# Kernel optimization log

Hardware: AMD Instinct MI355X
Metric: run time of the kernel (lower is better)

## Reference

```python
import jax, jax.numpy as jnp
import numpy as np

B, L, C, H, W = 2, 3, 64, 32, 32
DI, N, DT_RANK, K = 128, 16, 4, 4  # d_inner=2*C, d_state, dt_rank=ceil(C/16), 4 scan dirs


def setup_inputs() -> dict:
    key = jax.random.key(0)
    ks = iter(jax.random.split(key, 48))
    nrm = lambda shape, s=0.02: jax.random.normal(next(ks), shape, jnp.float32) * s
    return {
        "image_sequence": jax.random.normal(next(ks), (B, L, C, H, W), jnp.float32),
        "difficult_zone": jax.random.normal(next(ks), (B, C, H, W), jnp.float32),
        "sigma": jax.random.uniform(next(ks), (B, C, H, W), jnp.float32),
        # LayerNorm2d applied to each frame
        "norm_g": jnp.ones((C,)), "norm_b": jnp.zeros((C,)),
        # ConvolutionalResBlock (in=3C -> out=C), GroupNorm(num_groups=1)
        "gn1_g": jnp.ones((3 * C,)), "gn1_b": jnp.zeros((3 * C,)),
        "conv1_w": nrm((C, 3 * C, 3, 3)), "conv1_b": jnp.zeros((C,)),
        "gn2_g": jnp.ones((C,)), "gn2_b": jnp.zeros((C,)),
        "conv2_w": nrm((C, C, 3, 3)), "conv2_b": jnp.zeros((C,)),
        "skip_w": nrm((C, 3 * C, 1, 1)), "skip_b": jnp.zeros((C,)),
        # VSSBlock pre-norms
        "ln1_g": jnp.ones((C,)), "ln1_b": jnp.zeros((C,)),
        "ln2_g": jnp.ones((C,)), "ln2_b": jnp.zeros((C,)),
        # SS2D
        "in_proj_w": nrm((2 * DI, C)),
        "dwconv_w": nrm((DI, 1, 3, 3)), "dwconv_b": jnp.zeros((DI,)),
        "x_proj_w": nrm((K, DT_RANK + 2 * N, DI)),
        "dt_proj_w": nrm((K, DI, DT_RANK), 0.1),
        "dt_proj_b": jnp.log(jnp.expm1(jnp.full((K, DI), 0.01, jnp.float32))),
        "A_logs": jnp.log(jnp.tile(jnp.arange(1, N + 1, dtype=jnp.float32), (K * DI, 1))),
        "Ds": jnp.ones((K * DI,)),
        "out_norm_g": jnp.ones((DI,)), "out_norm_b": jnp.zeros((DI,)),
        "out_proj_w": nrm((C, DI)),
        # Mlp (hidden = C)
        "fc1_w": nrm((C, C)), "fc1_b": jnp.zeros((C,)),
        "fc2_w": nrm((C, C)), "fc2_b": jnp.zeros((C,)),
    }


def _ln(x, g, b, eps=1e-5):  # layernorm over last axis
    m = x.mean(-1, keepdims=True)
    v = x.var(-1, keepdims=True)
    return (x - m) * jax.lax.rsqrt(v + eps) * g + b


def _ln2d(x, g, b, eps=1e-6):  # per-pixel channel layernorm, NCHW
    m = x.mean(1, keepdims=True)
    v = x.var(1, keepdims=True)
    return (x - m) * jax.lax.rsqrt(v + eps) * g[None, :, None, None] + b[None, :, None, None]


def _gn1(x, g, b, eps=1e-5):  # GroupNorm(num_groups=1), NCHW
    m = x.mean((1, 2, 3), keepdims=True)
    v = x.var((1, 2, 3), keepdims=True)
    return (x - m) * jax.lax.rsqrt(v + eps) * g[None, :, None, None] + b[None, :, None, None]


def _conv(x, w, b, pad):
    y = jax.lax.conv_general_dilated(x, w, (1, 1), [(pad, pad), (pad, pad)],
                                     dimension_numbers=("NCHW", "OIHW", "NCHW"))
    return y + b[None, :, None, None]


def _forward(image_sequence, difficult_zone, sigma, norm_g, norm_b, gn1_g, gn1_b,
             conv1_w, conv1_b, gn2_g, gn2_b, conv2_w, conv2_b, skip_w, skip_b,
             ln1_g, ln1_b, ln2_g, ln2_b, in_proj_w, dwconv_w, dwconv_b, x_proj_w,
             dt_proj_w, dt_proj_b, A_logs, Ds, out_norm_g, out_norm_b, out_proj_w,
             fc1_w, fc1_b, fc2_w, fc2_b):
    b, l, c, h, w = image_sequence.shape
    bl, L2 = b * l, h * w
    # fold frame loop into batch (identical math per frame in the torch loop)
    frames = _ln2d(image_sequence.reshape(bl, c, h, w), norm_g, norm_b)
    dz = jnp.broadcast_to(difficult_zone[:, None], (b, l, c, h, w)).reshape(bl, c, h, w)
    sg = jnp.broadcast_to(sigma[:, None], (b, l, c, h, w)).reshape(bl, c, h, w)
    x = jnp.concatenate([dz, frames, sg], axis=1)  # [bl, 3c, h, w]
    # channel compressor: pre-act conv res block
    hdn = _conv(jax.nn.silu(_gn1(x, gn1_g, gn1_b)), conv1_w, conv1_b, 1)
    hdn = _conv(jax.nn.silu(_gn1(hdn, gn2_g, gn2_b)), conv2_w, conv2_b, 1)
    x = hdn + _conv(x, skip_w, skip_b, 0)          # [bl, c, h, w]
    x = x.transpose(0, 2, 3, 1)                    # [bl, h, w, c]
    # --- VSSBlock (pre-norm): x = x + SS2D(LN(x)) ---
    xn = _ln(x, ln1_g, ln1_b)
    xz = xn @ in_proj_w.T                          # [bl,h,w,2*DI]
    xc, z = jnp.split(xz, 2, axis=-1)
    xc = xc.transpose(0, 3, 1, 2)                  # [bl, DI, h, w]
    xc = jax.lax.conv_general_dilated(xc, dwconv_w, (1, 1), [(1, 1), (1, 1)],
                                      dimension_numbers=("NCHW", "OIHW", "NCHW"),
                                      feature_group_count=DI) + dwconv_b[None, :, None, None]
    xc = jax.nn.silu(xc)
    # 4-direction scan inputs (HW, WH, and their reverses)
    xf = xc.reshape(bl, DI, L2)
    xt = xc.transpose(0, 1, 3, 2).reshape(bl, DI, L2)
    xs = jnp.stack([xf, xt], axis=1)
    xs = jnp.concatenate([xs, jnp.flip(xs, axis=-1)], axis=1)  # [bl, 4, DI, L2]
    x_dbl = jnp.einsum("bkdl,kcd->bkcl", xs, x_proj_w)
    dts, Bs, Cs = jnp.split(x_dbl, [DT_RANK, DT_RANK + N], axis=2)
    dts = jnp.einsum("bkrl,kdr->bkdl", dts, dt_proj_w) + dt_proj_b[None, :, :, None]
    dts = jax.nn.softplus(dts)                     # [bl, 4, DI, L2]
    A = -jnp.exp(A_logs).reshape(K, DI, N)
    dA = jnp.exp(dts[..., None] * A[None, :, :, None, :])            # [bl,4,DI,L2,N]
    dBu = dts[..., None] * Bs.transpose(0, 1, 3, 2)[:, :, None] * xs[..., None]
    a_t = dA.transpose(3, 0, 1, 2, 4)              # [L2, bl, 4, DI, N]
    bu_t = dBu.transpose(3, 0, 1, 2, 4)
    c_t = Cs.transpose(3, 0, 1, 2)                 # [L2, bl, 4, N]

    def step(hid, inp):
        a_i, bu_i, c_i = inp
        hid = a_i * hid + bu_i
        return hid, jnp.einsum("bkdn,bkn->bkd", hid, c_i)

    h0 = jnp.zeros((bl, K, DI, N), xs.dtype)
    _, ys = jax.lax.scan(step, h0, (a_t, bu_t, c_t))                 # [L2, bl, 4, DI]
    ys = ys.transpose(1, 2, 3, 0) + xs * Ds.reshape(K, DI)[None, :, :, None]
    inv = jnp.flip(ys[:, 2:4], axis=-1)
    y = (ys[:, 0] + inv[:, 0]
         + ys[:, 1].reshape(bl, DI, w, h).transpose(0, 1, 3, 2).reshape(bl, DI, L2)
         + inv[:, 1].reshape(bl, DI, w, h).transpose(0, 1, 3, 2).reshape(bl, DI, L2))
    y = _ln(y.transpose(0, 2, 1), out_norm_g, out_norm_b).reshape(bl, h, w, DI)
    y = y * jax.nn.silu(z)
    x = x + y @ out_proj_w.T
    # --- x = x + Mlp(LN(x)) ---
    xn = _ln(x, ln2_g, ln2_b)
    x = x + (jax.nn.gelu(xn @ fc1_w.T + fc1_b, approximate=False) @ fc2_w.T + fc2_b)
    return x.transpose(0, 3, 1, 2).reshape(b, l, c, h, w)


def reference(image_sequence, difficult_zone, sigma, norm_g, norm_b, gn1_g, gn1_b,
              conv1_w, conv1_b, gn2_g, gn2_b, conv2_w, conv2_b, skip_w, skip_b,
              ln1_g, ln1_b, ln2_g, ln2_b, in_proj_w, dwconv_w, dwconv_b, x_proj_w,
              dt_proj_w, dt_proj_b, A_logs, Ds, out_norm_g, out_norm_b, out_proj_w,
              fc1_w, fc1_b, fc2_w, fc2_b):
    return _forward(image_sequence, difficult_zone, sigma, norm_g, norm_b, gn1_g, gn1_b,
                    conv1_w, conv1_b, gn2_g, gn2_b, conv2_w, conv2_b, skip_w, skip_b,
                    ln1_g, ln1_b, ln2_g, ln2_b, in_proj_w, dwconv_w, dwconv_b, x_proj_w,
                    dt_proj_w, dt_proj_b, A_logs, Ds, out_norm_g, out_norm_b, out_proj_w,
                    fc1_w, fc1_b, fc2_w, fc2_b)
```

## Files before the change

### kernel.cpp

```cpp
#include <hip/hip_runtime.h>
#include <math.h>

#define BL    6
#define CCH   64
#define C3    192
#define L2    1024
#define DIC   128
#define NST   16
#define K4    4
#define PSTR  1088
#define NCH   32

#define LOG2E 1.44269504088896340736f
#define LN2C  0.69314718055994530942f

__device__ __forceinline__ float fexp(float x){ return __builtin_amdgcn_exp2f(x*LOG2E); }
__device__ __forceinline__ float fsilu(float x){ return x / (1.f + fexp(-x)); }
__device__ __forceinline__ float fsoftplus(float x){
  if (x > 20.f) return x;
  return __builtin_amdgcn_logf(1.f + fexp(x)) * LN2C;
}
__device__ __forceinline__ float fgelu(float x){
  return 0.5f*x*(1.f + erff(x*0.70710678118654752440f));
}

__global__ __launch_bounds__(256) void k_ln2d(const float* __restrict__ img,
    const float* __restrict__ dz, const float* __restrict__ sg,
    const float* __restrict__ g, const float* __restrict__ b, float* __restrict__ x3c,
    float* __restrict__ psum1, float* __restrict__ psq1){
  __shared__ float ps[4][64], pq[4][64];
  int s = blockIdx.x >> 4;
  int lane = threadIdx.x & 63;
  int cg = threadIdx.x >> 6;
  int p = ((blockIdx.x & 15) << 6) + lane;
  int bsmp = s/3;
  const float* fr = img + (size_t)s*CCH*L2;
  float vals[16]; float sm=0.f, sq=0.f;
  #pragma unroll
  for (int j=0;j<16;++j){
    int c = cg*16+j;
    float v = fr[c*L2+p];
    vals[j]=v; sm+=v; sq+=v*v;
  }
  ps[cg][lane]=sm; pq[cg][lane]=sq;
  __syncthreads();
  sm = ps[0][lane]+ps[1][lane]+ps[2][lane]+ps[3][lane];
  sq = pq[0][lane]+pq[1][lane]+pq[2][lane]+pq[3][lane];
  float mean = sm*(1.f/CCH); float var = sq*(1.f/CCH) - mean*mean;
  float rs = rsqrtf(var + 1e-6f);
  float* o = x3c + (size_t)s*C3*L2;
  const float* dzp = dz + (size_t)bsmp*CCH*L2;
  const float* sgp = sg + (size_t)bsmp*CCH*L2;
  float gsm=0.f, gsq=0.f;
  #pragma unroll
  for (int j=0;j<16;++j){
    int c = cg*16+j;
    float dzv = dzp[c*L2+p];
    float nv  = (vals[j]-mean)*rs*g[c] + b[c];
    float sgv = sgp[c*L2+p];
    o[c*L2+p] = dzv;
    o[(CCH+c)*L2+p] = nv;
    o[(2*CCH+c)*L2+p] = sgv;
    gsm += dzv+nv+sgv; gsq += dzv*dzv+nv*nv+sgv*sgv;
  }
  for (int m=1;m<64;m<<=1){ gsm+=__shfl_xor(gsm,m,64); gsq+=__shfl_xor(gsq,m,64); }
  __syncthreads();
  if (lane==0){ ps[cg][0]=gsm; pq[cg][0]=gsq; }
  __syncthreads();
  if (threadIdx.x==0){
    atomicAdd(psum1+s, ps[0][0]+ps[1][0]+ps[2][0]+ps[3][0]);
    atomicAdd(psq1 +s, pq[0][0]+pq[1][0]+pq[2][0]+pq[3][0]);
  }
}

__global__ __launch_bounds__(256) void k_gnact_pad(const float* __restrict__ x,
    const float* __restrict__ psum, const float* __restrict__ psq,
    const float* __restrict__ g, const float* __restrict__ b,
    int ch, float inv_n, float eps, float* __restrict__ out){
  int bx = blockIdx.x;
  int s = bx / ch; int c = bx % ch;
  int tid = threadIdx.x;
  float mean = psum[s]*inv_n;
  float var = psq[s]*inv_n - mean*mean;
  float rs = rsqrtf(var + eps);
  float gc = g[c]*rs; float bc = b[c] - mean*rs*g[c];
  float4 v = *(const float4*)(x + (size_t)bx*1024 + tid*4);
  float4 o; o.x = fsilu(v.x*gc+bc); o.y = fsilu(v.y*gc+bc);
  o.z = fsilu(v.z*gc+bc); o.w = fsilu(v.w*gc+bc);
  float* pl = out + (size_t)bx*PSTR;
  *(float4*)(pl + 32 + tid*4) = o;
  float4 z4 = make_float4(0.f,0.f,0.f,0.f);
  if (tid < 8)  *(float4*)(pl + tid*4) = z4;
  else if (tid < 16) *(float4*)(pl + 1056 + (tid-8)*4) = z4;
}

__device__ __forceinline__ void conv_row_acc(float4& a0, float4& a1, float4 mid, float lf, float rt,
    const float* wp0, const float* wp1){
  float w0=wp0[0], w1=wp0[1], w2=wp0[2];
  a0.x = fmaf(w0,lf,   fmaf(w1,mid.x, fmaf(w2,mid.y, a0.x)));
  a0.y = fmaf(w0,mid.x,fmaf(w1,mid.y, fmaf(w2,mid.z, a0.y)));
  a0.z = fmaf(w0,mid.y,fmaf(w1,mid.z, fmaf(w2,mid.w, a0.z)));
  a0.w = fmaf(w0,mid.z,fmaf(w1,mid.w, fmaf(w2,rt,    a0.w)));
  float v0=wp1[0], v1=wp1[1], v2=wp1[2];
  a1.x = fmaf(v0,lf,   fmaf(v1,mid.x, fmaf(v2,mid.y, a1.x)));
  a1.y = fmaf(v0,mid.x,fmaf(v1,mid.y, fmaf(v2,mid.z, a1.y)));
  a1.z = fmaf(v0,mid.y,fmaf(v1,mid.z, fmaf(v2,mid.w, a1.z)));
  a1.w = fmaf(v0,mid.z,fmaf(v1,mid.w, fmaf(v2,rt,    a1.w)));
}

__device__ __forceinline__ void conv_ci_body(float4 m0, float4 m1, float4 m2, int q,
    const float* wp0, const float* wp1, float4& a0, float4& a1){
  float lf0=__shfl_up(m0.w,1,64), rt0=__shfl_down(m0.x,1,64);
  float lf1=__shfl_up(m1.w,1,64), rt1=__shfl_down(m1.x,1,64);
  float lf2=__shfl_up(m2.w,1,64), rt2=__shfl_down(m2.x,1,64);
  if (q==0){ lf0=0.f; lf1=0.f; lf2=0.f; }
  if (q==7){ rt0=0.f; rt1=0.f; rt2=0.f; }
  conv_row_acc(a0,a1,m0,lf0,rt0, wp0+0, wp1+0);
  conv_row_acc(a0,a1,m1,lf1,rt1, wp0+3, wp1+3);
  conv_row_acc(a0,a1,m2,lf2,rt2, wp0+6, wp1+6);
}

__global__ __launch_bounds__(256) void k_conv1_split(const float* __restrict__ xact,
    const float* __restrict__ w, float* __restrict__ part){
  int bx = blockIdx.x; int kk = bx&7; int cop=(bx>>3)&31; int s=bx>>8;
  int co0 = cop*2, co1 = co0+1;
  int tid = threadIdx.x; int row = tid>>3; int q = tid&7; int col0 = q*4;
  float4 a0 = make_float4(0.f,0.f,0.f,0.f);
  float4 a1 = make_float4(0.f,0.f,0.f,0.f);
  int ci0 = kk*24;
  const float* pl = xact + ((size_t)s*C3 + ci0)*PSTR + row*32 + col0;
  const float* wp0 = w + (size_t)(co0*C3 + ci0)*9;
  const float* wp1 = w + (size_t)(co1*C3 + ci0)*9;
  float4 m0 = *(const float4*)(pl);
  float4 m1 = *(const float4*)(pl+32);
  float4 m2 = *(const float4*)(pl+64);
  #pragma unroll 2
  for (int i=0;i<24;++i){
    const float* pn = pl + (i<23 ? PSTR : 0);
    float4 n0 = *(const float4*)(pn);
    float4 n1 = *(const float4*)(pn+32);
    float4 n2 = *(const float4*)(pn+64);
    conv_ci_body(m0,m1,m2,q, wp0, wp1, a0, a1);
    wp0 += 9; wp1 += 9; pl = pn; m0=n0; m1=n1; m2=n2;
  }
  float* pp = part + (size_t)kk*(BL*CCH*L2) + ((size_t)s*CCH+co0)*L2 + row*32+col0;
  *(float4*)pp = a0;
  *(float4*)(pp+L2) = a1;
}

__global__ __launch_bounds__(256) void k_reduce1(const float* __restrict__ part,
    const float* __restrict__ bias, float* __restrict__ h1,
    float* __restrict__ psum2, float* __restrict__ psq2){
  int co = blockIdx.x & 63; int s = blockIdx.x >> 6;
  size_t ofs = ((size_t)s*CCH+co)*L2 + threadIdx.x*4;
  const size_t stride = (size_t)BL*CCH*L2;
  float4 acc = *(const float4*)(part + ofs);
  #pragma unroll
  for (int kk=1;kk<8;++kk){
    float4 r = *(const float4*)(part + (size_t)kk*stride + ofs);
    acc.x += r.x; acc.y += r.y; acc.z += r.z; acc.w += r.w;
  }
  float bv = bias[co];
  acc.x += bv; acc.y += bv; acc.z += bv; acc.w += bv;
  *(float4*)(h1 + ofs) = acc;
  float sm = acc.x+acc.y+acc.z+acc.w;
  float sq = acc.x*acc.x+acc.y*acc.y+acc.z*acc.z+acc.w*acc.w;
  for (int m=1;m<64;m<<=1){ sm+=__shfl_xor(sm,m,64); sq+=__shfl_xor(sq,m,64); }
  __shared__ float s_sm[4], s_sq[4];
  int wv = threadIdx.x>>6;
  if ((threadIdx.x&63)==0){ s_sm[wv]=sm; s_sq[wv]=sq; }
  __syncthreads();
  if (threadIdx.x==0){
    atomicAdd(psum2+s, s_sm[0]+s_sm[1]+s_sm[2]+s_sm[3]);
    atomicAdd(psq2 +s, s_sq[0]+s_sq[1]+s_sq[2]+s_sq[3]);
  }
}

__global__ __launch_bounds__(256) void k_conv2_split(const float* __restrict__ xact2,
    const float* __restrict__ x3c, const float* __restrict__ w2,
    const float* __restrict__ wsk, float* __restrict__ part){
  int t = blockIdx.x; int role = t % 3; t /= 3;
  int cop = t & 31; int s = t >> 5;
  int co0 = cop*2, co1 = co0+1;
  int tid = threadIdx.x; int row = tid>>3; int q = tid&7; int col0 = q*4;
  int p = row*32+col0;
  float4 a0 = make_float4(0.f,0.f,0.f,0.f);
  float4 a1 = make_float4(0.f,0.f,0.f,0.f);
  if (role < 2){
    int ci0 = role*32;
    const float* pl = xact2 + ((size_t)s*CCH + ci0)*PSTR + row*32 + col0;
    const float* wp0 = w2 + (size_t)(co0*CCH + ci0)*9;
    const float* wp1 = w2 + (size_t)(co1*CCH + ci0)*9;
    float4 m0 = *(const float4*)(pl);
    float4 m1 = *(const float4*)(pl+32);
    float4 m2 = *(const float4*)(pl+64);
    #pragma unroll 2
    for (int i=0;i<32;++i){
      const float* pn = pl + (i<31 ? PSTR : 0);
      float4 n0 = *(const float4*)(pn);
      float4 n1 = *(const float4*)(pn+32);
      float4 n2 = *(const float4*)(pn+64);
      conv_ci_body(m0,m1,m2,q, wp0, wp1, a0, a1);
      wp0 += 9; wp1 += 9; pl = pn; m0=n0; m1=n1; m2=n2;
    }
  } else {
    const float* x3 = x3c + (size_t)s*C3*L2 + p;
    #pragma unroll 4
    for (int ci=0; ci<C3; ++ci){
      float4 v = *(const float4*)(x3 + (size_t)ci*L2);
      float ws0 = wsk[co0*C3+ci], ws1 = wsk[co1*C3+ci];
      a0.x = fmaf(ws0,v.x,a0.x); a0.y = fmaf(ws0,v.y,a0.y); a0.z = fmaf(ws0,v.z,a0.z); a0.w = fmaf(ws0,v.w,a0.w);
      a1.x = fmaf(ws1,v.x,a1.x); a1.y = fmaf(ws1,v.y,a1.y); a1.z = fmaf(ws1,v.z,a1.z); a1.w = fmaf(ws1,v.w,a1.w);
    }
  }
  float* pp = part + (size_t)role*(BL*CCH*L2) + ((size_t)s*CCH+co0)*L2 + p;
  *(float4*)pp = a0;
  *(float4*)(pp+L2) = a1;
}

__global__ __launch_bounds__(256) void k_reduce2(const float* __restrict__ part,
    const float* __restrict__ b2, const float* __restrict__ bsk,
    float* __restrict__ xp, float* __restrict__ x_cmaj){
  int co = blockIdx.x & 63; int s = blockIdx.x >> 6;
  int p = threadIdx.x*4;
  size_t ofs = ((size_t)s*CCH+co)*L2 + p;
  const size_t stride = (size_t)BL*CCH*L2;
  float4 r0 = *(const float4*)(part + ofs);
  float4 r1 = *(const float4*)(part + stride + ofs);
  float4 r2 = *(const float4*)(part + 2*stride + ofs);
  float bv = b2[co]+bsk[co];
  float4 o;
  o.x = r0.x+r1.x+r2.x+bv;
  o.y = r0.y+r1.y+r2.y+bv;
  o.z = r0.z+r1.z+r2.z+bv;
  o.w = r0.w+r1.w+r2.w+bv;
  *(float4*)(x_cmaj + ofs) = o;
  float* xpb = xp + ((size_t)s*L2 + p)*CCH + co;
  xpb[0] = o.x; xpb[CCH] = o.y; xpb[2*CCH] = o.z; xpb[3*CCH] = o.w;
}

__global__ __launch_bounds__(256) void k_ln1_inproj(const float* __restrict__ xp,
    const float* __restrict__ g, const float* __restrict__ b, const float* __restrict__ W,
    float* __restrict__ xc, float* __restrict__ z_t){
  __shared__ float xn_s[64*65];
  int bx = blockIdx.x; int oq = bx & 3; int pg = (bx>>2)&15; int s = bx>>6;
  int p0 = pg*64;
  int tid = threadIdx.x; int wv = __builtin_amdgcn_readfirstlane(tid>>6); int lane = tid&63;
  for (int j=0;j<16;++j){
    int pl = wv*16 + j; int p = p0 + pl;
    float v = xp[((size_t)s*L2 + p)*CCH + lane];
    float sm = v, sq = v*v;
    for (int m=1;m<64;m<<=1){ sm += __shfl_xor(sm,m,64); sq += __shfl_xor(sq,m,64); }
    float mean = sm*(1.f/64.f); float var = sq*(1.f/64.f) - mean*mean;
    float rs = rsqrtf(var + 1e-5f);
    xn_s[pl*65 + lane] = (v-mean)*rs*g[lane] + b[lane];
  }
  __syncthreads();
  int px_l = tid & 63;
  int og = __builtin_amdgcn_readfirstlane(tid >> 6);
  int o0 = oq*64 + og*16;
  float acc[16];
  #pragma unroll
  for (int oi=0;oi<16;++oi) acc[oi]=0.f;
  for (int c=0;c<64;++c){
    float xv = xn_s[px_l*65 + c];
    #pragma unroll
    for (int oi=0;oi<16;++oi) acc[oi] = fmaf(W[(o0+oi)*64 + c], xv, acc[oi]);
  }
  int p = p0 + px_l;
  if (oq < 2){
    #pragma unroll
    for (int oi=0;oi<16;++oi) xc[((size_t)s*DIC + o0 + oi)*L2 + p] = acc[oi];
  } else {
    #pragma unroll
    for (int oi=0;oi<16;++oi) z_t[((size_t)s*DIC + (o0-128) + oi)*L2 + p] = acc[oi];
  }
}

__global__ __launch_bounds__(256) void k_dwconv(const float* __restrict__ xc,
    const float* __restrict__ w, const float* __restrict__ bias, float* __restrict__ xconv){
  int bx = blockIdx.x; int dch = bx & 127; int s = bx >> 7;
  int tid = threadIdx.x; int row = tid>>3; int q = tid&7; int col0 = q*4;
  const float* xr = xc + ((size_t)s*DIC+dch)*L2;
  const float* wp = w + dch*9;
  float bv = bias[dch];
  float4 acc = make_float4(bv,bv,bv,bv);
  #pragma unroll
  for (int dy=-1;dy<=1;++dy){
    int r = row+dy;
    float4 mid = make_float4(0.f,0.f,0.f,0.f);
    if (0<=r && r<32) mid = *(const float4*)(xr + r*32 + col0);
    float lf = __shfl_up(mid.w,1,64); if(q==0) lf=0.f;
    float rt = __shfl_down(mid.x,1,64); if(q==7) rt=0.f;
    float w0=wp[(dy+1)*3], w1=wp[(dy+1)*3+1], w2=wp[(dy+1)*3+2];
    acc.x = fmaf(w0,lf,   fmaf(w1,mid.x, fmaf(w2,mid.y, acc.x)));
    acc.y = fmaf(w0,mid.x,fmaf(w1,mid.y, fmaf(w2,mid.z, acc.y)));
    acc.z = fmaf(w0,mid.y,fmaf(w1,mid.z, fmaf(w2,mid.w, acc.z)));
    acc.w = fmaf(w0,mid.z,fmaf(w1,mid.w, fmaf(w2,rt,    acc.w)));
  }
  acc.x = fsilu(acc.x); acc.y = fsilu(acc.y); acc.z = fsilu(acc.z); acc.w = fsilu(acc.w);
  *(float4*)(xconv + ((size_t)s*DIC+dch)*L2 + row*32+col0) = acc;
}

__global__ __launch_bounds__(256) void k_xproj_dt(const float* __restrict__ xconv,
    const float* __restrict__ W, const float* __restrict__ dtw, const float* __restrict__ dtb,
    float* __restrict__ dtp, float* __restrict__ Bp, float* __restrict__ Cp,
    float* __restrict__ u_t){
  __shared__ float smem[128*68];
  int bx = blockIdx.x; int pg = bx & 15; int sk = bx >> 4;
  int k = sk & 3; int s = sk >> 2;
  int tid = threadIdx.x;
  for (int i = tid; i < 128*16; i += 256){
    int dr = i>>4; int j4 = (i&15)*4;
    float4 v = *(const float4*)(xconv + ((size_t)(s*DIC + dr))*L2 + pg*64 + j4);
    *(float4*)&smem[dr*68 + j4] = v;
  }
  __syncthreads();
  if (k == 0){
    float* ub = u_t + ((size_t)(s*L2) + pg*64)*DIC;
    for (int i = tid; i < 64*128; i += 256){
      int px2 = i>>7; int dd = i&127;
      ub[(size_t)px2*DIC + dd] = smem[dd*68 + px2];
    }
  }
  int px = tid & 63;
  int cgrp = __builtin_amdgcn_readfirstlane(tid >> 6);
  int c0 = cgrp*9;
  const float* wb = W + (size_t)(k*36 + c0)*DIC;
  float acc[9];
  #pragma unroll
  for (int ci=0;ci<9;++ci) acc[ci]=0.f;
  for (int d=0; d<DIC; ++d){
    float xv = smem[d*68 + px];
    #pragma unroll
    for (int ci=0;ci<9;++ci) acc[ci] = fmaf(wb[ci*DIC+d], xv, acc[ci]);
  }
  __syncthreads();
  #pragma unroll
  for (int ci=0;ci<9;++ci) smem[(c0+ci)*68 + px] = acc[ci];
  __syncthreads();
  int d = tid & 127; int half = tid >> 7;
  float w0 = dtw[(k*DIC+d)*4+0], w1 = dtw[(k*DIC+d)*4+1];
  float w2 = dtw[(k*DIC+d)*4+2], w3 = dtw[(k*DIC+d)*4+3];
  float bb = dtb[k*DIC+d];
  float* dout = dtp + ((size_t)sk*L2 + pg*64)*DIC + d;
  for (int pp = half*32; pp < half*32+32; ++pp){
    float r0 = smem[0*68+pp], r1 = smem[1*68+pp], r2 = smem[2*68+pp], r3 = smem[3*68+pp];
    float val = fsoftplus(fmaf(w0,r0,fmaf(w1,r1,fmaf(w2,r2,fmaf(w3,r3,bb)))));
    dout[(size_t)pp*DIC] = val;
  }
  float* Bb = Bp + ((size_t)sk*L2 + pg*64)*NST;
  float* Cb = Cp + ((size_t)sk*L2 + pg*64)*NST;
  for (int i = tid; i < 1024; i += 256){
    int pp = i>>4; int n = i&15;
    Bb[pp*NST + n] = smem[(4+n)*68 + pp];
    Cb[pp*NST + n] = smem[(20+n)*68 + pp];
  }
}

__device__ __forceinline__ int scan_pix32(int ch, int j, int k){
  if (k==0) return ch*32 + j;
  if (k==1) return j*32 + ch;
  if (k==2) return 1023 - (ch*32 + j);
  return 1023 - (j*32 + ch);
}

struct StepB { float dtv, uv; float4 B0,B1,B2,B3; };
__device__ __forceinline__ StepB loadB(const float* db, const float* ub, const float* Bb, int p){
  StepB r;
  r.dtv = db[(size_t)p*DIC]; r.uv = ub[(size_t)p*DIC];
  const float* bp = Bb + p*NST;
  r.B0 = *(const float4*)bp; r.B1 = *(const float4*)(bp+4);
  r.B2 = *(const float4*)(bp+8); r.B3 = *(const float4*)(bp+12);
  return r;
}

__global__ __launch_bounds__(256,2) void k_scan_part3(const float* __restrict__ dtp,
    const float* __restrict__ u_t, const float* __restrict__ Bp,
    const float* __restrict__ A_logs, float* __restrict__ hend, float* __restrict__ prodA){
  int bx = blockIdx.x; int chp = bx & 15; int sk = bx >> 4;
  int k = sk & 3; int s = sk >> 2;
  int tid = threadIdx.x; int d = tid & 127; int ch = chp*2 + (tid>>7);
  float aco[16];
  {
    const float* ab = A_logs + (size_t)(k*DIC+d)*NST;
    #pragma unroll
    for (int n=0;n<16;++n) aco[n] = -LOG2E * fexp(ab[n]);
  }
  float h[16], Pr[16];
  #pragma unroll
  for (int n=0;n<16;++n){ h[n]=0.f; Pr[n]=1.f; }
  const float* db = dtp + (size_t)sk*L2*DIC + d;
  const float* ub = u_t + (size_t)s*L2*DIC + d;
  const float* Bb = Bp + (size_t)sk*L2*NST;
  StepB cur = loadB(db, ub, Bb, scan_pix32(ch, 0, k));
  #pragma unroll 4
  for (int j=0;j<32;++j){
    StepB nxt;
    if (j < 31) nxt = loadB(db, ub, Bb, scan_pix32(ch, j+1, k));
    float tv = cur.dtv*cur.uv;
    #define PSTEP(NI, BV) { float a_ = __builtin_amdgcn_exp2f(cur.dtv*aco[NI]); \
      h[NI] = fmaf(a_, h[NI], tv*(BV)); Pr[NI] *= a_; }
    PSTEP(0,cur.B0.x) PSTEP(1,cur.B0.y) PSTEP(2,cur.B0.z) PSTEP(3,cur.B0.w)
    PSTEP(4,cur.B1.x) PSTEP(5,cur.B1.y) PSTEP(6,cur.B1.z) PSTEP(7,cur.B1.w)
    PSTEP(8,cur.B2.x) PSTEP(9,cur.B2.y) PSTEP(10,cur.B2.z) PSTEP(11,cur.B2.w)
    PSTEP(12,cur.B3.x) PSTEP(13,cur.B3.y) PSTEP(14,cur.B3.z) PSTEP(15,cur.B3.w)
    #undef PSTEP
    cur = nxt;
  }
  size_t base = ((size_t)(sk*NCH + ch)*DIC + d)*NST;
  #pragma unroll
  for (int q4=0;q4<4;++q4){
    *(float4*)(hend + base + q4*4)  = make_float4(h[q4*4],h[q4*4+1],h[q4*4+2],h[q4*4+3]);
    *(float4*)(prodA + base + q4*4) = make_float4(Pr[q4*4],Pr[q4*4+1],Pr[q4*4+2],Pr[q4*4+3]);
  }
}

__global__ __launch_bounds__(256) void k_scan_fix3(const float* __restrict__ hend,
    float* prodA_Hin){
  int t = blockIdx.x*256 + threadIdx.x;
  int n = t & 15; int d = (t>>4) & 127; int sk = t >> 11;
  float H = 0.f;
  for (int ch=0; ch<NCH; ++ch){
    size_t idx = ((size_t)(sk*NCH + ch)*DIC + d)*NST + n;
    float pa = prodA_Hin[idx];
    float he = hend[idx];
    prodA_Hin[idx] = H;
    H = fmaf(pa, H, he);
  }
}

__global__ __launch_bounds__(256,2) void k_scan_y3(const float* __restrict__ dtp,
    const float* __restrict__ u_t, const float* __restrict__ Bp, const float* __restrict__ Cp,
    const float* __restrict__ A_logs, const float* __restrict__ Ds,
    const float* __restrict__ Hin, float* __restrict__ ys_t){
  int bx = blockIdx.x; int chp = bx & 15; int sk = bx >> 4;
  int k = sk & 3; int s = sk >> 2;
  int tid = threadIdx.x; int d = tid & 127; int ch = chp*2 + (tid>>7);
  float aco[16];
  {
    const float* ab = A_logs + (size_t)(k*DIC+d)*NST;
    #pragma unroll
    for (int n=0;n<16;++n) aco[n] = -LOG2E * fexp(ab[n]);
  }
  float Dv = Ds[k*DIC+d];
  float h[16];
  size_t hbase = ((size_t)(sk*NCH + ch)*DIC + d)*NST;
  #pragma unroll
  for (int q4=0;q4<4;++q4){
    float4 hv = *(const float4*)(Hin + hbase + q4*4);
    h[q4*4]=hv.x; h[q4*4+1]=hv.y; h[q4*4+2]=hv.z; h[q4*4+3]=hv.w;
  }
  const float* db = dtp + (size_t)sk*L2*DIC + d;
  const float* ub = u_t + (size_t)s*L2*DIC + d;
  const float* Bb = Bp + (size_t)sk*L2*NST;
  const float* Cb = Cp + (size_t)sk*L2*NST;
  float* yb = ys_t + (size_t)sk*L2*DIC + d;
  int pcur = scan_pix32(ch, 0, k);
  StepB cur = loadB(db, ub, Bb, pcur);
  float4 Cc0 = *(const float4*)(Cb + pcur*NST);
  float4 Cc1 = *(const float4*)(Cb + pcur*NST + 4);
  float4 Cc2 = *(const float4*)(Cb + pcur*NST + 8);
  float4 Cc3 = *(const float4*)(Cb + pcur*NST + 12);
  #pragma unroll 4
  for (int j=0;j<32;++j){
    StepB nxt; float4 Cn0, Cn1, Cn2, Cn3; int pn = pcur;
    if (j < 31){
      pn = scan_pix32(ch, j+1, k);
      nxt = loadB(db, ub, Bb, pn);
      Cn0 = *(const float4*)(Cb + pn*NST);
      Cn1 = *(const float4*)(Cb + pn*NST + 4);
      Cn2 = *(const float4*)(Cb + pn*NST + 8);
      Cn3 = *(const float4*)(Cb + pn*NST + 12);
    }
    float tv = cur.dtv*cur.uv;
    float y0=0.f, y1=0.f, y2=0.f, y3=0.f;
    #define YSTEP(NI, BV, CV, YA) { float a_ = __builtin_amdgcn_exp2f(cur.dtv*aco[NI]); \
      h[NI] = fmaf(a_, h[NI], tv*(BV)); YA = fmaf(h[NI], (CV), YA); }
    YSTEP(0,cur.B0.x,Cc0.x,y0) YSTEP(1,cur.B0.y,Cc0.y,y1) YSTEP(2,cur.B0.z,Cc0.z,y2) YSTEP(3,cur.B0.w,Cc0.w,y3)
    YSTEP(4,cur.B1.x,Cc1.x,y0) YSTEP(5,cur.B1.y,Cc1.y,y1) YSTEP(6,cur.B1.z,Cc1.z,y2) YSTEP(7,cur.B1.w,Cc1.w,y3)
    YSTEP(8,cur.B2.x,Cc2.x,y0) YSTEP(9,cur.B2.y,Cc2.y,y1) YSTEP(10,cur.B2.z,Cc2.z,y2) YSTEP(11,cur.B2.w,Cc2.w,y3)
    YSTEP(12,cur.B3.x,Cc3.x,y0) YSTEP(13,cur.B3.y,Cc3.y,y1) YSTEP(14,cur.B3.z,Cc3.z,y2) YSTEP(15,cur.B3.w,Cc3.w,y3)
    #undef YSTEP
    yb[(size_t)pcur*DIC] = fmaf(cur.uv, Dv, (y0+y1)+(y2+y3));
    cur = nxt; Cc0 = Cn0; Cc1 = Cn1; Cc2 = Cn2; Cc3 = Cn3; pcur = pn;
  }
}

__global__ __launch_bounds__(256) void k_combine_outproj(const float* __restrict__ ys_t,
    const float* __restrict__ z_t, const float* __restrict__ g, const float* __restrict__ b,
    const float* __restrict__ W, const float* __restrict__ x_cmaj, float* __restrict__ xv){
  __shared__ float yt[128*17];
  int s = blockIdx.x >> 6; int pg = blockIdx.x & 63;
  int tid = threadIdx.x;
  int wv = __builtin_amdgcn_readfirstlane(tid>>6); int lane = tid&63;
  int d0 = lane, d1 = lane+64;
  for (int i=0;i<4;++i){
    int px = i*4 + wv; int p = pg*16 + px;
    const float* yb = ys_t + ((size_t)(s*4)*L2 + p)*DIC;
    float ya = yb[d0] + yb[(size_t)L2*DIC + d0] + yb[(size_t)2*L2*DIC + d0] + yb[(size_t)3*L2*DIC + d0];
    float yc = yb[d1] + yb[(size_t)L2*DIC + d1] + yb[(size_t)2*L2*DIC + d1] + yb[(size_t)3*L2*DIC + d1];
    float sm = ya+yc, sq = ya*ya+yc*yc;
    for (int m=1;m<64;m<<=1){ sm+=__shfl_xor(sm,m,64); sq+=__shfl_xor(sq,m,64); }
    float mean = sm*(1.f/128.f); float var = sq*(1.f/128.f)-mean*mean;
    float rs = rsqrtf(var + 1e-5f);
    float yn0 = (ya-mean)*rs*g[d0] + b[d0];
    float yn1 = (yc-mean)*rs*g[d1] + b[d1];
    float zv0 = z_t[((size_t)s*DIC+d0)*L2 + p];
    float zv1 = z_t[((size_t)s*DIC+d1)*L2 + p];
    yt[d0*17 + px] = yn0 * fsilu(zv0);
    yt[d1*17 + px] = yn1 * fsilu(zv1);
  }
  __syncthreads();
  int px = tid & 15; int cg = tid >> 4;
  int c0 = cg*4;
  float a0=0.f,a1=0.f,a2=0.f,a3=0.f;
  for (int d=0; d<DIC; ++d){
    float yv = yt[d*17 + px];
    a0 = fmaf(W[(c0+0)*DIC + d], yv, a0);
    a1 = fmaf(W[(c0+1)*DIC + d], yv, a1);
    a2 = fmaf(W[(c0+2)*DIC + d], yv, a2);
    a3 = fmaf(W[(c0+3)*DIC + d], yv, a3);
  }
  int p = pg*16 + px;
  size_t base = ((size_t)s*CCH + c0)*L2 + p;
  xv[base]      = x_cmaj[base]      + a0;
  xv[base+L2]   = x_cmaj[base+L2]   + a1;
  xv[base+2*L2] = x_cmaj[base+2*L2] + a2;
  xv[base+3*L2] = x_cmaj[base+3*L2] + a3;
}

__global__ __launch_bounds__(256) void k_mlp(const float* __restrict__ xv_in,
    const float* __restrict__ g, const float* __restrict__ b,
    const float* __restrict__ w1, const float* __restrict__ b1,
    const float* __restrict__ w2, const float* __restrict__ b2, float* __restrict__ out){
  __shared__ float xt[64*33];
  __shared__ float ts[32*65];
  int s = blockIdx.x >> 5; int p0 = (blockIdx.x & 31)*32;
  int tid = threadIdx.x; int px = tid & 31; int cg = tid >> 5;
  #pragma unroll
  for (int j=0;j<8;++j){
    int c = cg*8 + j;
    xt[c*33 + px] = xv_in[((size_t)s*CCH + c)*L2 + p0 + px];
  }
  __syncthreads();
  float sm=0.f, sq=0.f;
  for (int c=0;c<64;++c){ float v = xt[c*33+px]; sm+=v; sq+=v*v; }
  float mean = sm*(1.f/64.f);
  float rs = rsqrtf(sq*(1.f/64.f) - mean*mean + 1e-5f);
  int o0 = cg*8;
  float t[8];
  #pragma unroll
  for (int oi=0;oi<8;++oi) t[oi] = b1[o0+oi];
  for (int c=0;c<64;++c){
    float xn = (xt[c*33+px]-mean)*rs*g[c] + b[c];
    #pragma unroll
    for (int oi=0;oi<8;++oi) t[oi] = fmaf(xn, w1[(o0+oi)*64 + c], t[oi]);
  }
  #pragma unroll
  for (int oi=0;oi<8;++oi) ts[px*65 + o0+oi] = fgelu(t[oi]);
  __syncthreads();
  int c0 = cg*8;
  float acc[8];
  #pragma unroll
  for (int ci=0;ci<8;++ci) acc[ci] = xt[(c0+ci)*33+px] + b2[c0+ci];
  for (int o=0;o<64;++o){
    float tv = ts[px*65 + o];
    #pragma unroll
    for (int ci=0;ci<8;++ci) acc[ci] = fmaf(tv, w2[(c0+ci)*64 + o], acc[ci]);
  }
  #pragma unroll
  for (int ci=0;ci<8;++ci) out[((size_t)s*CCH + c0+ci)*L2 + p0 + px] = acc[ci];
}

extern "C" void kernel_launch(void* const* d_in, const int* in_sizes, int n_in,
                              void* d_out, int out_size, void* d_ws, size_t ws_size,
                              hipStream_t stream){
  (void)in_sizes; (void)n_in; (void)out_size; (void)ws_size;
  const float* img      = (const float*)d_in[0];
  const float* dz       = (const float*)d_in[1];
  const float* sg       = (const float*)d_in[2];
  const float* norm_g   = (const float*)d_in[3];
  const float* norm_b   = (const float*)d_in[4];
  const float* gn1_g    = (const float*)d_in[5];
  const float* gn1_b    = (const float*)d_in[6];
  const float* conv1_w  = (const float*)d_in[7];
  const float* conv1_b  = (const float*)d_in[8];
  const float* gn2_g    = (const float*)d_in[9];
  const float* gn2_b    = (const float*)d_in[10];
  const float* conv2_w  = (const float*)d_in[11];
  const float* conv2_b  = (const float*)d_in[12];
  const float* skip_w   = (const float*)d_in[13];
  const float* skip_b   = (const float*)d_in[14];
  const float* ln1_g    = (const float*)d_in[15];
  const float* ln1_b    = (const float*)d_in[16];
  const float* ln2_g    = (const float*)d_in[17];
  const float* ln2_b    = (const float*)d_in[18];
  const float* in_proj_w= (const float*)d_in[19];
  const float* dwconv_w = (const float*)d_in[20];
  const float* dwconv_b = (const float*)d_in[21];
  const float* x_proj_w = (const float*)d_in[22];
  const float* dt_proj_w= (const float*)d_in[23];
  const float* dt_proj_b= (const float*)d_in[24];
  const float* A_logs   = (const float*)d_in[25];
  const float* Ds       = (const float*)d_in[26];
  const float* out_norm_g = (const float*)d_in[27];
  const float* out_norm_b = (const float*)d_in[28];
  const float* out_proj_w = (const float*)d_in[29];
  const float* fc1_w    = (const float*)d_in[30];
  const float* fc1_b    = (const float*)d_in[31];
  const float* fc2_w    = (const float*)d_in[32];
  const float* fc2_b    = (const float*)d_in[33];

  float* ws = (float*)d_ws;
  float* x3c    = ws;
  float* xact1  = x3c    + 1179648;
  float* h1     = xact1  + 1253376;
  float* xact2  = h1     + 393216;
  float* xp     = xact2  + 417792;
  float* x_cmaj = xp     + 393216;
  float* z_t    = x_cmaj + 393216;
  float* xc     = z_t    + 786432;
  float* xconv  = xc     + 786432;
  float* hole   = xconv  + 786432;
  float* dtp    = hole   + 884736;
  float* ys_t   = dtp    + 3145728;
  float* xv     = ys_t   + 3145728;
  float* statsb = xv     + 393216;
  float* psum1  = statsb;
  float* psq1   = statsb + 6;
  float* psum2  = statsb + 12;
  float* psq2   = statsb + 18;
  float* part1  = dtp;
  float* part2  = ys_t;
  float* hend   = x3c;
  float* prodA  = xconv;
  float* u_t    = h1;
  float* Bp     = xp;
  float* Cp     = xc;

  hipMemsetAsync(statsb, 0, 24*sizeof(float), stream);
  k_ln2d<<<96, 256, 0, stream>>>(img, dz, sg, norm_g, norm_b, x3c, psum1, psq1);
  k_gnact_pad<<<6*C3, 256, 0, stream>>>(x3c, psum1, psq1, gn1_g, gn1_b, C3,
                                        1.f/(C3*L2), 1e-5f, xact1);
  k_conv1_split<<<1536, 256, 0, stream>>>(xact1, conv1_w, part1);
  k_reduce1<<<384, 256, 0, stream>>>(part1, conv1_b, h1, psum2, psq2);
  k_gnact_pad<<<6*CCH, 256, 0, stream>>>(h1, psum2, psq2, gn2_g, gn2_b, CCH,
                                         1.f/(CCH*L2), 1e-5f, xact2);
  k_conv2_split<<<576, 256, 0, stream>>>(xact2, x3c, conv2_w, skip_w, part2);
  k_reduce2<<<384, 256, 0, stream>>>(part2, conv2_b, skip_b, xp, x_cmaj);
  k_ln1_inproj<<<384, 256, 0, stream>>>(xp, ln1_g, ln1_b, in_proj_w, xc, z_t);
  k_dwconv<<<768, 256, 0, stream>>>(xc, dwconv_w, dwconv_b, xconv);
  k_xproj_dt<<<384, 256, 0, stream>>>(xconv, x_proj_w, dt_proj_w, dt_proj_b, dtp, Bp, Cp, u_t);
  k_scan_part3<<<384, 256, 0, stream>>>(dtp, u_t, Bp, A_logs, hend, prodA);
  k_scan_fix3<<<192, 256, 0, stream>>>(hend, prodA);
  k_scan_y3<<<384, 256, 0, stream>>>(dtp, u_t, Bp, Cp, A_logs, Ds, prodA, ys_t);
  k_combine_outproj<<<384, 256, 0, stream>>>(ys_t, z_t, out_norm_g, out_norm_b,
                                             out_proj_w, x_cmaj, xv);
  k_mlp<<<192, 256, 0, stream>>>(xv, ln2_g, ln2_b, fc1_w, fc1_b, fc2_w, fc2_b, (float*)d_out);
}
```

Measured before the change: 316.8 us.

## Fuse out-projection with MLP tail and replace stat atomics with per-block partials

Merges the combine/out-projection kernel and the MLP kernel into one kernel that keeps the residual tile in shared memory, removing a global round trip for xv and one launch. GroupNorm statistics are now written as per-block partial sums and reduced by each consumer block, instead of being accumulated with atomics into a buffer that needed a memset first. The memset call goes away, at the cost of every gnact block re-reading 16 or 64 partials. The fused kernel computes the MLP for 16 pixels per block with 4 channels per thread, down from 32 pixels with 8 channels per thread.

```diff
diff --git a/kernel.cpp b/kernel.cpp
--- a/kernel.cpp
+++ b/kernel.cpp
@@ -68,20 +68,22 @@
   if (lane==0){ ps[cg][0]=gsm; pq[cg][0]=gsq; }
   __syncthreads();
   if (threadIdx.x==0){
-    atomicAdd(psum1+s, ps[0][0]+ps[1][0]+ps[2][0]+ps[3][0]);
-    atomicAdd(psq1 +s, pq[0][0]+pq[1][0]+pq[2][0]+pq[3][0]);
+    psum1[blockIdx.x] = ps[0][0]+ps[1][0]+ps[2][0]+ps[3][0];
+    psq1 [blockIdx.x] = pq[0][0]+pq[1][0]+pq[2][0]+pq[3][0];
   }
 }
 
 __global__ __launch_bounds__(256) void k_gnact_pad(const float* __restrict__ x,
     const float* __restrict__ psum, const float* __restrict__ psq,
     const float* __restrict__ g, const float* __restrict__ b,
-    int ch, float inv_n, float eps, float* __restrict__ out){
+    int ch, int parts, float inv_n, float eps, float* __restrict__ out){
   int bx = blockIdx.x;
   int s = bx / ch; int c = bx % ch;
   int tid = threadIdx.x;
-  float mean = psum[s]*inv_n;
-  float var = psq[s]*inv_n - mean*mean;
+  float sm=0.f, sq=0.f;
+  for (int i=0;i<parts;++i){ sm += psum[s*parts+i]; sq += psq[s*parts+i]; }
+  float mean = sm*inv_n;
+  float var = sq*inv_n - mean*mean;
   float rs = rsqrtf(var + eps);
   float gc = g[c]*rs; float bc = b[c] - mean*rs*g[c];
   float4 v = *(const float4*)(x + (size_t)bx*1024 + tid*4);
@@ -171,8 +173,8 @@
   if ((threadIdx.x&63)==0){ s_sm[wv]=sm; s_sq[wv]=sq; }
   __syncthreads();
   if (threadIdx.x==0){
-    atomicAdd(psum2+s, s_sm[0]+s_sm[1]+s_sm[2]+s_sm[3]);
-    atomicAdd(psq2 +s, s_sq[0]+s_sq[1]+s_sq[2]+s_sq[3]);
+    psum2[blockIdx.x] = s_sm[0]+s_sm[1]+s_sm[2]+s_sm[3];
+    psq2 [blockIdx.x] = s_sq[0]+s_sq[1]+s_sq[2]+s_sq[3];
   }
 }
 
@@ -487,90 +489,87 @@
   }
 }
 
-__global__ __launch_bounds__(256) void k_combine_outproj(const float* __restrict__ ys_t,
-    const float* __restrict__ z_t, const float* __restrict__ g, const float* __restrict__ b,
-    const float* __restrict__ W, const float* __restrict__ x_cmaj, float* __restrict__ xv){
+__global__ __launch_bounds__(256) void k_tail(const float* __restrict__ ys_t,
+    const float* __restrict__ z_t, const float* __restrict__ ong, const float* __restrict__ onb,
+    const float* __restrict__ Wop, const float* __restrict__ x_cmaj,
+    const float* __restrict__ g2, const float* __restrict__ b2n,
+    const float* __restrict__ w1, const float* __restrict__ b1,
+    const float* __restrict__ w2, const float* __restrict__ b2,
+    float* __restrict__ out){
   __shared__ float yt[128*17];
+  __shared__ float xvt[64*17];
+  __shared__ float ts[64*17];
   int s = blockIdx.x >> 6; int pg = blockIdx.x & 63;
   int tid = threadIdx.x;
-  int wv = __builtin_amdgcn_readfirstlane(tid>>6); int lane = tid&63;
-  int d0 = lane, d1 = lane+64;
-  for (int i=0;i<4;++i){
-    int px = i*4 + wv; int p = pg*16 + px;
-    const float* yb = ys_t + ((size_t)(s*4)*L2 + p)*DIC;
-    float ya = yb[d0] + yb[(size_t)L2*DIC + d0] + yb[(size_t)2*L2*DIC + d0] + yb[(size_t)3*L2*DIC + d0];
-    float yc = yb[d1] + yb[(size_t)L2*DIC + d1] + yb[(size_t)2*L2*DIC + d1] + yb[(size_t)3*L2*DIC + d1];
-    float sm = ya+yc, sq = ya*ya+yc*yc;
-    for (int m=1;m<64;m<<=1){ sm+=__shfl_xor(sm,m,64); sq+=__shfl_xor(sq,m,64); }
-    float mean = sm*(1.f/128.f); float var = sq*(1.f/128.f)-mean*mean;
-    float rs = rsqrtf(var + 1e-5f);
-    float yn0 = (ya-mean)*rs*g[d0] + b[d0];
-    float yn1 = (yc-mean)*rs*g[d1] + b[d1];
-    float zv0 = z_t[((size_t)s*DIC+d0)*L2 + p];
-    float zv1 = z_t[((size_t)s*DIC+d1)*L2 + p];
-    yt[d0*17 + px] = yn0 * fsilu(zv0);
-    yt[d1*17 + px] = yn1 * fsilu(zv1);
-  }
-  __syncthreads();
-  int px = tid & 15; int cg = tid >> 4;
-  int c0 = cg*4;
-  float a0=0.f,a1=0.f,a2=0.f,a3=0.f;
-  for (int d=0; d<DIC; ++d){
-    float yv = yt[d*17 + px];
-    a0 = fmaf(W[(c0+0)*DIC + d], yv, a0);
-    a1 = fmaf(W[(c0+1)*DIC + d], yv, a1);
-    a2 = fmaf(W[(c0+2)*DIC + d], yv, a2);
-    a3 = fmaf(W[(c0+3)*DIC + d], yv, a3);
-  }
-  int p = pg*16 + px;
-  size_t base = ((size_t)s*CCH + c0)*L2 + p;
-  xv[base]      = x_cmaj[base]      + a0;
-  xv[base+L2]   = x_cmaj[base+L2]   + a1;
-  xv[base+2*L2] = x_cmaj[base+2*L2] + a2;
-  xv[base+3*L2] = x_cmaj[base+3*L2] + a3;
-}
-
-__global__ __launch_bounds__(256) void k_mlp(const float* __restrict__ xv_in,
-    const float* __restrict__ g, const float* __restrict__ b,
-    const float* __restrict__ w1, const float* __restrict__ b1,
-    const float* __restrict__ w2, const float* __restrict__ b2, float* __restrict__ out){
-  __shared__ float xt[64*33];
-  __shared__ float ts[32*65];
-  int s = blockIdx.x >> 5; int p0 = (blockIdx.x & 31)*32;
-  int tid = threadIdx.x; int px = tid & 31; int cg = tid >> 5;
-  #pragma unroll
-  for (int j=0;j<8;++j){
-    int c = cg*8 + j;
-    xt[c*33 + px] = xv_in[((size_t)s*CCH + c)*L2 + p0 + px];
-  }
-  __syncthreads();
+  {
+    int wv = __builtin_amdgcn_readfirstlane(tid>>6); int lane = tid&63;
+    int d0 = lane, d1 = lane+64;
+    for (int i=0;i<4;++i){
+      int px = i*4 + wv; int p = pg*16 + px;
+      const float* yb = ys_t + ((size_t)(s*4)*L2 + p)*DIC;
+      float ya = yb[d0] + yb[(size_t)L2*DIC + d0] + yb[(size_t)2*L2*DIC + d0] + yb[(size_t)3*L2*DIC + d0];
+      float yc = yb[d1] + yb[(size_t)L2*DIC + d1] + yb[(size_t)2*L2*DIC + d1] + yb[(size_t)3*L2*DIC + d1];
+      float sm = ya+yc, sq = ya*ya+yc*yc;
+      for (int m=1;m<64;m<<=1){ sm+=__shfl_xor(sm,m,64); sq+=__shfl_xor(sq,m,64); }
+      float mean = sm*(1.f/128.f); float var = sq*(1.f/128.f)-mean*mean;
+      float rs = rsqrtf(var + 1e-5f);
+      float yn0 = (ya-mean)*rs*ong[d0] + onb[d0];
+      float yn1 = (yc-mean)*rs*ong[d1] + onb[d1];
+      float zv0 = z_t[((size_t)s*DIC+d0)*L2 + p];
+      float zv1 = z_t[((size_t)s*DIC+d1)*L2 + p];
+      yt[d0*17 + px] = yn0 * fsilu(zv0);
+      yt[d1*17 + px] = yn1 * fsilu(zv1);
+    }
+  }
+  __syncthreads();
+  {
+    int px = tid & 15; int cgp = tid >> 4;
+    int c0 = cgp*4;
+    float a0=0.f,a1=0.f,a2=0.f,a3=0.f;
+    for (int d=0; d<DIC; ++d){
+      float yv = yt[d*17 + px];
+      a0 = fmaf(Wop[(c0+0)*DIC + d], yv, a0);
+      a1 = fmaf(Wop[(c0+1)*DIC + d], yv, a1);
+      a2 = fmaf(Wop[(c0+2)*DIC + d], yv, a2);
+      a3 = fmaf(Wop[(c0+3)*DIC + d], yv, a3);
+    }
+    int p = pg*16 + px;
+    size_t base = ((size_t)s*CCH + c0)*L2 + p;
+    xvt[(c0+0)*17 + px] = x_cmaj[base]      + a0;
+    xvt[(c0+1)*17 + px] = x_cmaj[base+L2]   + a1;
+    xvt[(c0+2)*17 + px] = x_cmaj[base+2*L2] + a2;
+    xvt[(c0+3)*17 + px] = x_cmaj[base+3*L2] + a3;
+  }
+  __syncthreads();
+  int px = tid & 15; int cgp = tid >> 4;
   float sm=0.f, sq=0.f;
-  for (int c=0;c<64;++c){ float v = xt[c*33+px]; sm+=v; sq+=v*v; }
+  for (int c=0;c<64;++c){ float v = xvt[c*17+px]; sm+=v; sq+=v*v; }
   float mean = sm*(1.f/64.f);
   float rs = rsqrtf(sq*(1.f/64.f) - mean*mean + 1e-5f);
-  int o0 = cg*8;
-  float t[8];
-  #pragma unroll
-  for (int oi=0;oi<8;++oi) t[oi] = b1[o0+oi];
+  int o0 = cgp*4;
+  float t[4];
+  #pragma unroll
+  for (int oi=0;oi<4;++oi) t[oi] = b1[o0+oi];
   for (int c=0;c<64;++c){
-    float xn = (xt[c*33+px]-mean)*rs*g[c] + b[c];
-    #pragma unroll
-    for (int oi=0;oi<8;++oi) t[oi] = fmaf(xn, w1[(o0+oi)*64 + c], t[oi]);
-  }
-  #pragma unroll
-  for (int oi=0;oi<8;++oi) ts[px*65 + o0+oi] = fgelu(t[oi]);
-  __syncthreads();
-  int c0 = cg*8;
-  float acc[8];
-  #pragma unroll
-  for (int ci=0;ci<8;++ci) acc[ci] = xt[(c0+ci)*33+px] + b2[c0+ci];
+    float xn = (xvt[c*17+px]-mean)*rs*g2[c] + b2n[c];
+    #pragma unroll
+    for (int oi=0;oi<4;++oi) t[oi] = fmaf(xn, w1[(o0+oi)*64 + c], t[oi]);
+  }
+  #pragma unroll
+  for (int oi=0;oi<4;++oi) ts[(o0+oi)*17 + px] = fgelu(t[oi]);
+  __syncthreads();
+  int c0 = cgp*4;
+  float acc[4];
+  #pragma unroll
+  for (int ci=0;ci<4;++ci) acc[ci] = xvt[(c0+ci)*17+px] + b2[c0+ci];
   for (int o=0;o<64;++o){
-    float tv = ts[px*65 + o];
-    #pragma unroll
-    for (int ci=0;ci<8;++ci) acc[ci] = fmaf(tv, w2[(c0+ci)*64 + o], acc[ci]);
-  }
-  #pragma unroll
-  for (int ci=0;ci<8;++ci) out[((size_t)s*CCH + c0+ci)*L2 + p0 + px] = acc[ci];
+    float tv = ts[o*17+px];
+    #pragma unroll
+    for (int ci=0;ci<4;++ci) acc[ci] = fmaf(tv, w2[(c0+ci)*64 + o], acc[ci]);
+  }
+  int p = pg*16 + px;
+  #pragma unroll
+  for (int ci=0;ci<4;++ci) out[((size_t)s*CCH + c0+ci)*L2 + p] = acc[ci];
 }
 
 extern "C" void kernel_launch(void* const* d_in, const int* in_sizes, int n_in,
@@ -625,12 +624,11 @@
   float* hole   = xconv  + 786432;
   float* dtp    = hole   + 884736;
   float* ys_t   = dtp    + 3145728;
-  float* xv     = ys_t   + 3145728;
-  float* statsb = xv     + 393216;
+  float* statsb = ys_t   + 3145728;
   float* psum1  = statsb;
-  float* psq1   = statsb + 6;
-  float* psum2  = statsb + 12;
-  float* psq2   = statsb + 18;
+  float* psq1   = statsb + 96;
+  float* psum2  = statsb + 192;
+  float* psq2   = statsb + 576;
   float* part1  = dtp;
   float* part2  = ys_t;
   float* hend   = x3c;
@@ -639,13 +637,12 @@
   float* Bp     = xp;
   float* Cp     = xc;
 
-  hipMemsetAsync(statsb, 0, 24*sizeof(float), stream);
   k_ln2d<<<96, 256, 0, stream>>>(img, dz, sg, norm_g, norm_b, x3c, psum1, psq1);
-  k_gnact_pad<<<6*C3, 256, 0, stream>>>(x3c, psum1, psq1, gn1_g, gn1_b, C3,
+  k_gnact_pad<<<6*C3, 256, 0, stream>>>(x3c, psum1, psq1, gn1_g, gn1_b, C3, 16,
                                         1.f/(C3*L2), 1e-5f, xact1);
   k_conv1_split<<<1536, 256, 0, stream>>>(xact1, conv1_w, part1);
   k_reduce1<<<384, 256, 0, stream>>>(part1, conv1_b, h1, psum2, psq2);
-  k_gnact_pad<<<6*CCH, 256, 0, stream>>>(h1, psum2, psq2, gn2_g, gn2_b, CCH,
+  k_gnact_pad<<<6*CCH, 256, 0, stream>>>(h1, psum2, psq2, gn2_g, gn2_b, CCH, 64,
                                          1.f/(CCH*L2), 1e-5f, xact2);
   k_conv2_split<<<576, 256, 0, stream>>>(xact2, x3c, conv2_w, skip_w, part2);
   k_reduce2<<<384, 256, 0, stream>>>(part2, conv2_b, skip_b, xp, x_cmaj);
@@ -655,7 +652,6 @@
   k_scan_part3<<<384, 256, 0, stream>>>(dtp, u_t, Bp, A_logs, hend, prodA);
   k_scan_fix3<<<192, 256, 0, stream>>>(hend, prodA);
   k_scan_y3<<<384, 256, 0, stream>>>(dtp, u_t, Bp, Cp, A_logs, Ds, prodA, ys_t);
-  k_combine_outproj<<<384, 256, 0, stream>>>(ys_t, z_t, out_norm_g, out_norm_b,
-                                             out_proj_w, x_cmaj, xv);
-  k_mlp<<<192, 256, 0, stream>>>(xv, ln2_g, ln2_b, fc1_w, fc1_b, fc2_w, fc2_b, (float*)d_out);
-}
+  k_tail<<<384, 256, 0, stream>>>(ys_t, z_t, out_norm_g, out_norm_b, out_proj_w, x_cmaj,
+                                  ln2_g, ln2_b, fc1_w, fc1_b, fc2_w, fc2_b, (float*)d_out);
+}
```

New measurement: 308.6 us. 1.03x faster.
